# Optimization experiments

Measured on AMD Instinct MI355X. Metric: run time of the kernel, lower is better.

Reference implementation:

```python
import jax, jax.numpy as jnp
import numpy as np

BN_EPS = 1e-5


def setup_inputs() -> dict:
    key = jax.random.key(0)
    ks = jax.random.split(key, 7)
    C, Cb = 512, 128
    B, H, W = 32, 64, 64
    inp = jax.random.normal(ks[0], (B, C, H, W), dtype=jnp.float32)
    # 1x1 conv == linear over channels; kaiming-ish init scale
    w1 = jax.random.normal(ks[1], (Cb, C), dtype=jnp.float32) * (1.0 / np.sqrt(C))
    b1 = jax.random.normal(ks[2], (Cb,), dtype=jnp.float32) * 0.01
    gamma = jnp.ones((Cb,), dtype=jnp.float32)
    beta = jnp.zeros((Cb,), dtype=jnp.float32)
    w2 = jax.random.normal(ks[3], (C, Cb), dtype=jnp.float32) * (1.0 / np.sqrt(Cb))
    b2 = jax.random.normal(ks[4], (C,), dtype=jnp.float32) * 0.01
    return {"input": inp, "w1": w1, "b1": b1, "gamma": gamma, "beta": beta,
            "w2": w2, "b2": b2}


def reference(input, w1, b1, gamma, beta, w2, b2):
    # squeeze: global average pool over H,W -> [B, C]
    s = jnp.mean(input, axis=(2, 3))
    # 1x1 conv (channels -> bottleneck) + ReLU
    h = jax.nn.relu(jnp.einsum("bc,kc->bk", s, w1) + b1)  # [B, Cb]
    # BatchNorm2d on [B, Cb, 1, 1] in training mode: stats over batch dim
    mu = jnp.mean(h, axis=0)
    var = jnp.var(h, axis=0)  # biased, matches torch BN normalization
    h = (h - mu) * jax.lax.rsqrt(var + BN_EPS) * gamma + beta
    # 1x1 conv (bottleneck -> channels) + sigmoid gate
    g = jax.nn.sigmoid(jnp.einsum("bk,ck->bc", h, w2) + b2)  # [B, C]
    # excite: broadcast multiply
    return input * g[:, :, None, None]
```

## Files before the change

### kernel.cpp

```cpp
#include <hip/hip_runtime.h>
#include <math.h>

#define CC 512
#define CB 128
#define BB 32
#define HW 4096

typedef float f32x4 __attribute__((ext_vector_type(4)));

__global__ __launch_bounds__(256) void se_pool(const float* __restrict__ in,
                                               float* __restrict__ s) {
    int bc = blockIdx.x;
    const f32x4* row = (const f32x4*)(in + (size_t)bc * HW);
    int t = threadIdx.x;
    float acc = 0.f;
#pragma unroll
    for (int i = 0; i < 4; ++i) {
        f32x4 v = row[t + i * 256];
        acc += v.x + v.y + v.z + v.w;
    }
#pragma unroll
    for (int off = 32; off >= 1; off >>= 1)
        acc += __shfl_xor(acc, off, 64);
    __shared__ float red[4];
    if ((t & 63) == 0) red[t >> 6] = acc;
    __syncthreads();
    if (t == 0) {
        s[bc] = (red[0] + red[1] + red[2] + red[3]) * (1.0f / HW);
    }
}

__global__ __launch_bounds__(256) void se_h(const float* __restrict__ s,
                                            const float* __restrict__ w1,
                                            const float* __restrict__ b1,
                                            float* __restrict__ h) {
    int k = blockIdx.x;
    __shared__ float wrow[CC];
    int t = threadIdx.x;
    wrow[t]       = w1[k * CC + t];
    wrow[t + 256] = w1[k * CC + t + 256];
    __syncthreads();
    int b = t >> 3;
    int p = t & 7;
    const float* srow = s + b * CC + p * 64;
    const float* wp   = wrow + p * 64;
    float acc = 0.f;
#pragma unroll
    for (int j = 0; j < 64; ++j) acc += srow[j] * wp[j];
    acc += __shfl_xor(acc, 1, 64);
    acc += __shfl_xor(acc, 2, 64);
    acc += __shfl_xor(acc, 4, 64);
    if (p == 0) {
        float v = acc + b1[k];
        h[b * CB + k] = v > 0.f ? v : 0.f;
    }
}

__global__ __launch_bounds__(128) void se_bn(float* __restrict__ h,
                                             const float* __restrict__ gamma,
                                             const float* __restrict__ beta) {
    int k = threadIdx.x;
    float sum = 0.f, sumsq = 0.f;
#pragma unroll
    for (int b = 0; b < BB; ++b) {
        float v = h[b * CB + k];
        sum += v;
        sumsq += v * v;
    }
    float mu  = sum * (1.0f / BB);
    float var = sumsq * (1.0f / BB) - mu * mu;
    float sc  = gamma[k] * rsqrtf(var + 1e-5f);
    float sh  = beta[k] - mu * sc;
#pragma unroll
    for (int b = 0; b < BB; ++b)
        h[b * CB + k] = h[b * CB + k] * sc + sh;
}

__global__ __launch_bounds__(256) void se_mul(const float* __restrict__ in,
                                              const float* __restrict__ hn,
                                              const float* __restrict__ w2,
                                              const float* __restrict__ b2,
                                              float* __restrict__ out) {
    int bc = (BB * CC - 1) - blockIdx.x;
    int b = bc >> 9;
    int c = bc & 511;
    const f32x4* hv = (const f32x4*)(hn + b * CB);
    const f32x4* wv = (const f32x4*)(w2 + c * CB);
    float acc = 0.f;
#pragma unroll
    for (int i = 0; i < 32; ++i) {
        f32x4 a = hv[i];
        f32x4 w = wv[i];
        acc += a.x * w.x + a.y * w.y + a.z * w.z + a.w * w.w;
    }
    float g = 1.0f / (1.0f + expf(-(acc + b2[c])));

    const f32x4* iv = (const f32x4*)(in + (size_t)bc * HW);
    f32x4* ov       = (f32x4*)(out + (size_t)bc * HW);
    int t = threadIdx.x;
#pragma unroll
    for (int i = 0; i < 4; ++i) {
        f32x4 v = iv[t + i * 256];
        v.x *= g; v.y *= g; v.z *= g; v.w *= g;
        __builtin_nontemporal_store(v, &ov[t + i * 256]);
    }
}

extern "C" void kernel_launch(void* const* d_in, const int* in_sizes, int n_in,
                              void* d_out, int out_size, void* d_ws, size_t ws_size,
                              hipStream_t stream) {
    const float* in    = (const float*)d_in[0];
    const float* w1    = (const float*)d_in[1];
    const float* b1    = (const float*)d_in[2];
    const float* gamma = (const float*)d_in[3];
    const float* beta  = (const float*)d_in[4];
    const float* w2    = (const float*)d_in[5];
    const float* b2    = (const float*)d_in[6];
    float* out = (float*)d_out;

    float* s = (float*)d_ws;
    float* h = s + BB * CC;

    se_pool<<<BB * CC, 256, 0, stream>>>(in, s);
    se_h<<<CB, 256, 0, stream>>>(s, w1, b1, h);
    se_bn<<<1, CB, 0, stream>>>(h, gamma, beta);
    se_mul<<<BB * CC, 256, 0, stream>>>(in, h, w2, b2, out);
}
```

Before: 128.4 us.

## Fuse SE into one cooperative kernel keeping input on-chip as bf16

Replaces the four-kernel pipeline with a single cooperative kernel. Each block pools 32 rows and keeps its slice of the input on-chip as bf16, 7 rows in LDS and the rest in registers. Grid syncs separate the FC1+BN stage from the FC2+sigmoid gate, and the output is then written from the on-chip copy. This is meant to remove the second full HBM read of the input and the extra launches. In exchange it loses precision, since outputs are computed from bf16-rounded inputs, and it relies on heavy register and LDS use so that all 512 blocks can be co-resident. If the cooperative launch fails, it falls back to the old kernels.

```diff
diff --git a/kernel.cpp b/kernel.cpp
--- a/kernel.cpp
+++ b/kernel.cpp
@@ -1,12 +1,155 @@
 #include <hip/hip_runtime.h>
+#include <hip/hip_cooperative_groups.h>
 #include <math.h>
 
 #define CC 512
 #define CB 128
 #define BB 32
 #define HW 4096
+#define NROW (BB * CC)
+#define ROWS_PB 32
+#define NBLK (NROW / ROWS_PB)
+#define NTHR 256
+#define LDSROWS 7
+#define REGROWS (ROWS_PB - LDSROWS)
+#define CHUNKS 4
 
 typedef float f32x4 __attribute__((ext_vector_type(4)));
+typedef unsigned short u16x4 __attribute__((ext_vector_type(4)));
+
+static __device__ __forceinline__ unsigned short f2bf(float x) {
+    unsigned u = __float_as_uint(x);
+    unsigned r = (u + 0x7fffu + ((u >> 16) & 1u)) >> 16;
+    return (unsigned short)r;
+}
+static __device__ __forceinline__ float bf2f(unsigned short b) {
+    return __uint_as_float(((unsigned)b) << 16);
+}
+
+__global__ __launch_bounds__(NTHR, 2) void se_fused(
+    const float* __restrict__ in, const float* __restrict__ w1,
+    const float* __restrict__ b1, const float* __restrict__ gamma,
+    const float* __restrict__ beta, const float* __restrict__ w2,
+    const float* __restrict__ b2, float* __restrict__ out,
+    float* __restrict__ s, float* __restrict__ hn)
+{
+    __shared__ unsigned short ldat[LDSROWS * HW];
+    __shared__ float redbuf[ROWS_PB][4];
+    __shared__ float hrow[BB];
+    __shared__ float grow[ROWS_PB];
+
+    const int t   = threadIdx.x;
+    const int blk = blockIdx.x;
+    const int R0  = blk * ROWS_PB;
+    const int wv  = t >> 6, ln = t & 63;
+
+    u16x4 dreg[REGROWS * CHUNKS];
+
+#pragma unroll
+    for (int lr = 0; lr < ROWS_PB; ++lr) {
+        const f32x4* rp = (const f32x4*)(in + (size_t)(R0 + lr) * HW);
+        float part = 0.f;
+#pragma unroll
+        for (int j = 0; j < CHUNKS; ++j) {
+            f32x4 v = rp[t + j * NTHR];
+            part += v.x + v.y + v.z + v.w;
+            u16x4 cv;
+            cv.x = f2bf(v.x); cv.y = f2bf(v.y); cv.z = f2bf(v.z); cv.w = f2bf(v.w);
+            if (lr < LDSROWS) {
+                *(u16x4*)&ldat[lr * HW + (t + j * NTHR) * 4] = cv;
+            } else {
+                dreg[(lr - LDSROWS) * CHUNKS + j] = cv;
+            }
+        }
+#pragma unroll
+        for (int off = 32; off >= 1; off >>= 1)
+            part += __shfl_xor(part, off, 64);
+        if (ln == 0) redbuf[lr][wv] = part;
+    }
+    __syncthreads();
+    if (t < ROWS_PB) {
+        float sum = redbuf[t][0] + redbuf[t][1] + redbuf[t][2] + redbuf[t][3];
+        s[R0 + t] = sum * (1.0f / HW);
+    }
+    __threadfence();
+    cooperative_groups::this_grid().sync();
+
+    if (blk < CB) {
+        const int k = blk;
+        const int b = t >> 3, p = t & 7;
+        const f32x4* sr = (const f32x4*)(s  + b * CC + p * 64);
+        const f32x4* wr = (const f32x4*)(w1 + k * CC + p * 64);
+        float acc = 0.f;
+#pragma unroll
+        for (int j = 0; j < 16; ++j) {
+            f32x4 a = sr[j], w = wr[j];
+            acc += a.x * w.x + a.y * w.y + a.z * w.z + a.w * w.w;
+        }
+        acc += __shfl_xor(acc, 1, 64);
+        acc += __shfl_xor(acc, 2, 64);
+        acc += __shfl_xor(acc, 4, 64);
+        if (p == 0) {
+            float v = acc + b1[k];
+            hrow[b] = v > 0.f ? v : 0.f;
+        }
+        __syncthreads();
+        if (t == 0) {
+            float su = 0.f, sq = 0.f;
+            for (int bb = 0; bb < BB; ++bb) { float v = hrow[bb]; su += v; sq += v * v; }
+            float mu  = su * (1.0f / BB);
+            float var = sq * (1.0f / BB) - mu * mu;
+            redbuf[0][0] = mu;
+            redbuf[0][1] = gamma[k] * rsqrtf(var + 1e-5f);
+        }
+        __syncthreads();
+        if (t < BB) {
+            float mu = redbuf[0][0], sc = redbuf[0][1];
+            hn[t * CB + k] = (hrow[t] - mu) * sc + beta[k];
+        }
+    }
+    __threadfence();
+    cooperative_groups::this_grid().sync();
+
+    {
+        const int r = t >> 3, p = t & 7;
+        const int R = R0 + r;
+        const int bb = R >> 9, cc = R & 511;
+        const f32x4* hr = (const f32x4*)(hn + bb * CB + p * 16);
+        const f32x4* wr = (const f32x4*)(w2 + cc * CB + p * 16);
+        float acc = 0.f;
+#pragma unroll
+        for (int j = 0; j < 4; ++j) {
+            f32x4 a = hr[j], w = wr[j];
+            acc += a.x * w.x + a.y * w.y + a.z * w.z + a.w * w.w;
+        }
+        acc += __shfl_xor(acc, 1, 64);
+        acc += __shfl_xor(acc, 2, 64);
+        acc += __shfl_xor(acc, 4, 64);
+        if (p == 0) grow[r] = 1.0f / (1.0f + expf(-(acc + b2[cc])));
+    }
+    __syncthreads();
+
+#pragma unroll
+    for (int lr = 0; lr < ROWS_PB; ++lr) {
+        float g = grow[lr];
+        f32x4* op = (f32x4*)(out + (size_t)(R0 + lr) * HW);
+#pragma unroll
+        for (int j = 0; j < CHUNKS; ++j) {
+            u16x4 cv;
+            if (lr < LDSROWS) {
+                cv = *(const u16x4*)&ldat[lr * HW + (t + j * NTHR) * 4];
+            } else {
+                cv = dreg[(lr - LDSROWS) * CHUNKS + j];
+            }
+            f32x4 v;
+            v.x = bf2f(cv.x) * g;
+            v.y = bf2f(cv.y) * g;
+            v.z = bf2f(cv.z) * g;
+            v.w = bf2f(cv.w) * g;
+            __builtin_nontemporal_store(v, &op[t + j * NTHR]);
+        }
+    }
+}
 
 __global__ __launch_bounds__(256) void se_pool(const float* __restrict__ in,
                                                float* __restrict__ s) {
@@ -25,9 +168,7 @@
     __shared__ float red[4];
     if ((t & 63) == 0) red[t >> 6] = acc;
     __syncthreads();
-    if (t == 0) {
-        s[bc] = (red[0] + red[1] + red[2] + red[3]) * (1.0f / HW);
-    }
+    if (t == 0) s[bc] = (red[0] + red[1] + red[2] + red[3]) * (1.0f / HW);
 }
 
 __global__ __launch_bounds__(256) void se_h(const float* __restrict__ s,
@@ -40,8 +181,7 @@
     wrow[t]       = w1[k * CC + t];
     wrow[t + 256] = w1[k * CC + t + 256];
     __syncthreads();
-    int b = t >> 3;
-    int p = t & 7;
+    int b = t >> 3, p = t & 7;
     const float* srow = s + b * CC + p * 64;
     const float* wp   = wrow + p * 64;
     float acc = 0.f;
@@ -64,8 +204,7 @@
 #pragma unroll
     for (int b = 0; b < BB; ++b) {
         float v = h[b * CB + k];
-        sum += v;
-        sumsq += v * v;
+        sum += v; sumsq += v * v;
     }
     float mu  = sum * (1.0f / BB);
     float var = sumsq * (1.0f / BB) - mu * mu;
@@ -81,20 +220,17 @@
                                               const float* __restrict__ w2,
                                               const float* __restrict__ b2,
                                               float* __restrict__ out) {
-    int bc = (BB * CC - 1) - blockIdx.x;
-    int b = bc >> 9;
-    int c = bc & 511;
+    int bc = (NROW - 1) - blockIdx.x;
+    int b = bc >> 9, c = bc & 511;
     const f32x4* hv = (const f32x4*)(hn + b * CB);
     const f32x4* wv = (const f32x4*)(w2 + c * CB);
     float acc = 0.f;
 #pragma unroll
     for (int i = 0; i < 32; ++i) {
-        f32x4 a = hv[i];
-        f32x4 w = wv[i];
+        f32x4 a = hv[i], w = wv[i];
         acc += a.x * w.x + a.y * w.y + a.z * w.z + a.w * w.w;
     }
     float g = 1.0f / (1.0f + expf(-(acc + b2[c])));
-
     const f32x4* iv = (const f32x4*)(in + (size_t)bc * HW);
     f32x4* ov       = (f32x4*)(out + (size_t)bc * HW);
     int t = threadIdx.x;
@@ -118,11 +254,19 @@
     const float* b2    = (const float*)d_in[6];
     float* out = (float*)d_out;
 
-    float* s = (float*)d_ws;
-    float* h = s + BB * CC;
-
-    se_pool<<<BB * CC, 256, 0, stream>>>(in, s);
-    se_h<<<CB, 256, 0, stream>>>(s, w1, b1, h);
-    se_bn<<<1, CB, 0, stream>>>(h, gamma, beta);
-    se_mul<<<BB * CC, 256, 0, stream>>>(in, h, w2, b2, out);
-}
+    float* s  = (float*)d_ws;
+    float* hn = s + NROW;
+
+    void* args[] = { (void*)&in, (void*)&w1, (void*)&b1, (void*)&gamma,
+                     (void*)&beta, (void*)&w2, (void*)&b2, (void*)&out,
+                     (void*)&s, (void*)&hn };
+    hipError_t e = hipLaunchCooperativeKernel((const void*)se_fused,
+                                              dim3(NBLK), dim3(NTHR),
+                                              args, 0, stream);
+    if (e != hipSuccess) {
+        se_pool<<<NROW, 256, 0, stream>>>(in, s);
+        se_h<<<CB, 256, 0, stream>>>(s, w1, b1, hn);
+        se_bn<<<1, CB, 0, stream>>>(hn, gamma, beta);
+        se_mul<<<NROW, 256, 0, stream>>>(in, hn, w2, b2, out);
+    }
+}
```

Measured after the change: 342.5 us. 2.67x slower.
